# Kernel optimization log

Hardware: AMD Instinct MI355X
Metric: run time of the kernel (lower is better)

The kernel has to match this reference:

```python
import jax, jax.numpy as jnp
import numpy as np

B, T, D, NC = 2048, 16, 2048, 174
DH = D // 2
EPS = 1e-5


def setup_inputs() -> dict:
    key = jax.random.key(0)
    ks = jax.random.split(key, 10)
    std = 0.01
    return {
        "x": jax.random.normal(ks[0], (B, T, D), dtype=jnp.float32),
        "theta_w": jax.random.normal(ks[1], (DH, D), dtype=jnp.float32) * std,
        "phi_w": jax.random.normal(ks[2], (DH, D), dtype=jnp.float32) * std,
        "g_w": jax.random.normal(ks[3], (DH, D), dtype=jnp.float32) * std,
        "W_w": jax.random.normal(ks[4], (D, DH), dtype=jnp.float32) * std,
        "bn_gamma": jnp.ones((D,), dtype=jnp.float32),
        "bn_beta": jnp.zeros((D,), dtype=jnp.float32),
        "bn_mean": jax.random.normal(ks[5], (D,), dtype=jnp.float32) * 0.1,
        "bn_var": jax.random.uniform(ks[6], (D,), dtype=jnp.float32, minval=0.5, maxval=1.5),
        "fc1_w": jax.random.normal(ks[7], (512, T * D), dtype=jnp.float32) * 0.01,
        "fc1_b": jnp.zeros((512,), dtype=jnp.float32),
        "fc2_w": jax.random.normal(ks[8], (NC, 512), dtype=jnp.float32) * 0.01,
        "fc2_b": jnp.zeros((NC,), dtype=jnp.float32),
    }


def _bn(x_bdt, gamma, beta, mean, var):
    # inference-mode BatchNorm1d over channel dim D of [B, D, T]
    inv = gamma / jnp.sqrt(var + EPS)
    return x_bdt * inv[None, :, None] + (beta - mean * inv)[None, :, None]


def _attention_net(x_btd, theta_w, phi_w, g_w, W_w, bn):
    x_bdt = x_btd.reshape(B, D, T)  # torch .view semantics (reshape, not transpose)
    theta_x = jnp.einsum('od,bdt->bot', theta_w, x_bdt)  # [B, DH, T]
    phi_x = jnp.einsum('od,bdt->bot', phi_w, x_bdt)
    g_x = jnp.einsum('od,bdt->bot', g_w, x_bdt)
    scores = jnp.einsum('bot,bos->bts', theta_x, phi_x) / DH  # [B, T, T]
    alpha = jax.nn.softmax(scores, axis=-1)  # dropout is identity in eval
    context = jnp.einsum('bts,bos->bto', alpha, g_x)  # [B, T, DH]
    ctx = jnp.einsum('do,bto->bdt', W_w, context)  # W 1x1 conv -> [B, D, T]
    ctx = _bn(ctx, *bn)
    ctx = ctx.reshape(B, T, D)  # view(B, shape[-1], shape[-2])
    return ctx + x_btd


def _residual_block(x_bdt, theta_w, phi_w, g_w, W_w, bn):
    y = x_bdt
    h = _bn(x_bdt, *bn)
    h = h.reshape(B, T, D)
    h = _attention_net(h, theta_w, phi_w, g_w, W_w, bn)
    h = h.reshape(B, D, T)
    h = _bn(h, *bn)
    return h + y


def reference(x, theta_w, phi_w, g_w, W_w, bn_gamma, bn_beta, bn_mean, bn_var,
              fc1_w, fc1_b, fc2_w, fc2_b):
    bn = (bn_gamma, bn_beta, bn_mean, bn_var)
    skip = x  # [B, T, D]
    h = x.reshape(B, D, T)
    for _ in range(T):  # num_frames residual blocks (shared weights)
        h = _residual_block(h, theta_w, phi_w, g_w, W_w, bn)
    h = _bn(h, *bn)
    h = h.reshape(B, T, D) + skip
    h = h.reshape(B, T * D)
    h = jax.nn.relu(h)
    h = jax.nn.relu(h @ fc1_w.T + fc1_b)  # trn dropout identity in eval
    return h @ fc2_w.T + fc2_b  # [B, num_class]
```

## Files before the change

### kernel.cpp

```cpp
#include <hip/hip_runtime.h>
#include <math.h>
#include <stdint.h>


typedef float  floatx4 __attribute__((ext_vector_type(4)));
typedef float  floatx2 __attribute__((ext_vector_type(2)));
typedef _Float16 half8 __attribute__((ext_vector_type(8)));
typedef short  short8 __attribute__((ext_vector_type(8)));
typedef unsigned short ushort2v __attribute__((ext_vector_type(2)));
typedef unsigned short ushort4v __attribute__((ext_vector_type(4)));

#define BIGK (1 << 28)

__device__ __forceinline__ unsigned short h_bits(_Float16 h) {
  return __builtin_bit_cast(unsigned short, h);
}

__device__ __forceinline__ void gld_lds16(const unsigned short* g, unsigned short* l) {
  __builtin_amdgcn_global_load_lds(
      (const __attribute__((address_space(1))) unsigned int*)g,
      (__attribute__((address_space(3))) unsigned int*)l, 16, 0, 0);
}

template <int EPI>
__global__ __launch_bounds__(256, 2)
void gemm_f16(const unsigned short* __restrict__ A, int lda, int kfA,
              const unsigned short* __restrict__ B, int ldb, int kfB,
              int K, float* __restrict__ out0, unsigned short* __restrict__ out1,
              int ldo, const float* __restrict__ tbl,
              float cmult, float uscale, int writeU, long zAB, long zO) {
  __shared__ unsigned short As[128 * 64];
  __shared__ unsigned short Bs[128 * 64];
  if (zAB) { A += (long)blockIdx.z * zAB; B += (long)blockIdx.z * zAB; }
  if (zO) { out0 += (long)blockIdx.z * zO; }
  const int tid = threadIdx.x;
  const int w = tid >> 6, l = tid & 63;
  const int quad = l >> 4, lr = l & 15;
  const int m0 = blockIdx.x * 128, n0 = blockIdx.y * 128;
  const int wm = (w & 1) * 64, wn = (w >> 1) * 64;
  const int lsw = lr & 7;

  floatx4 acc[4][4];
#pragma unroll
  for (int a = 0; a < 4; a++)
#pragma unroll
    for (int b = 0; b < 4; b++)
#pragma unroll
      for (int q = 0; q < 4; q++) acc[a][b][q] = 0.f;

  for (int k0 = 0; k0 < K; k0 += 64) {
    int ka = (k0 >= kfA) ? k0 - kfA : k0;
    int kb = (k0 >= kfB) ? k0 - kfB : k0;
    __syncthreads();
#pragma unroll
    for (int i = 0; i < 4; i++) {
      int c = i * 256 + tid;
      int m = c >> 3;
      int kc = ((c & 7) ^ (m & 7)) * 8;
      gld_lds16(A + (size_t)(m0 + m) * lda + ka + kc, As + c * 8);
      gld_lds16(B + (size_t)(n0 + m) * ldb + kb + kc, Bs + c * 8);
    }
    __syncthreads();
#pragma unroll
    for (int kk = 0; kk < 64; kk += 32) {
      const int kq = (kk >> 3) + quad;
      const int ksw = (kq ^ lsw) * 8;
      short8 af[4], bf[4];
#pragma unroll
      for (int mi = 0; mi < 4; mi++)
        af[mi] = *(const short8*)(As + (wm + mi * 16 + lr) * 64 + ksw);
#pragma unroll
      for (int ni = 0; ni < 4; ni++)
        bf[ni] = *(const short8*)(Bs + (wn + ni * 16 + lr) * 64 + ksw);
#pragma unroll
      for (int mi = 0; mi < 4; mi++)
#pragma unroll
        for (int ni = 0; ni < 4; ni++)
          acc[mi][ni] = __builtin_amdgcn_mfma_f32_16x16x32_f16(
              __builtin_bit_cast(half8, af[mi]),
              __builtin_bit_cast(half8, bf[ni]), acc[mi][ni], 0, 0, 0);
    }
  }

  if (EPI == 0) {
#pragma unroll
    for (int mi = 0; mi < 4; mi++)
#pragma unroll
      for (int i2 = 0; i2 < 4; i2++) {
        int row = m0 + wm + mi * 16 + quad * 4 + i2;
#pragma unroll
        for (int ni = 0; ni < 4; ni++) {
          int col = n0 + wn + ni * 16 + lr;
          out0[(size_t)row * ldo + col] = acc[mi][ni][i2];
        }
      }
  } else {
    float invv[4], bb[4];
#pragma unroll
    for (int ni = 0; ni < 4; ni++) {
      int d = n0 + wn + ni * 16 + lr;
      invv[ni] = tbl[d];
      bb[ni] = tbl[2048 + d];
    }
#pragma unroll
    for (int mi = 0; mi < 4; mi++)
#pragma unroll
      for (int i2 = 0; i2 < 4; i2++) {
        size_t row = (size_t)(m0 + wm + mi * 16 + quad * 4 + i2);
#pragma unroll
        for (int ni = 0; ni < 4; ni++) {
          int d = n0 + wn + ni * 16 + lr;
          size_t off = row * (size_t)ldo + d;
          float hold = out0[off];
          float ctxv = acc[mi][ni][i2] * cmult;
          float u = __fadd_rn(__fmul_rn(hold, invv[ni]), bb[ni]);
          float cb = __fadd_rn(__fmul_rn(ctxv, invv[ni]), bb[ni]);
          float o1 = __fadd_rn(cb, u);
          float h2 = __fadd_rn(__fmul_rn(o1, invv[ni]), bb[ni]);
          float hn = __fadd_rn(h2, hold);
          out0[off] = hn;
          float un = __fadd_rn(__fmul_rn(hn, invv[ni]), bb[ni]);
          acc[mi][ni][i2] = un * uscale;
        }
      }
    if (writeU) {
      unsigned short* st = (w < 2) ? (As + w * 4096) : (Bs + (w - 2) * 4096);
      __syncthreads();
#pragma unroll
      for (int mi = 0; mi < 4; mi++)
#pragma unroll
        for (int i2 = 0; i2 < 4; i2++) {
          int rr = mi * 16 + quad * 4 + i2;
#pragma unroll
          for (int ni = 0; ni < 4; ni++)
            st[rr * 64 + ni * 16 + lr] = h_bits((_Float16)acc[mi][ni][i2]);
        }
      __syncthreads();
#pragma unroll
      for (int j = 0; j < 8; j++) {
        int chk = j * 64 + l, rr = chk >> 3, c8 = (chk & 7) * 8;
        short8 v = *(const short8*)(st + rr * 64 + c8);
        *(short8*)(out1 + (size_t)(m0 + wm + rr) * (2 * ldo) + n0 + wn + c8) = v;
      }
      __syncthreads();
#pragma unroll
      for (int mi = 0; mi < 4; mi++)
#pragma unroll
        for (int i2 = 0; i2 < 4; i2++) {
          int rr = mi * 16 + quad * 4 + i2;
#pragma unroll
          for (int ni = 0; ni < 4; ni++) {
            float u = acc[mi][ni][i2];
            _Float16 hh = (_Float16)u;
            st[rr * 64 + ni * 16 + lr] = h_bits((_Float16)(u - (float)hh));
          }
        }
      __syncthreads();
#pragma unroll
      for (int j = 0; j < 8; j++) {
        int chk = j * 64 + l, rr = chk >> 3, c8 = (chk & 7) * 8;
        short8 v = *(const short8*)(st + rr * 64 + c8);
        *(short8*)(out1 + (size_t)(m0 + wm + rr) * (2 * ldo) + ldo + n0 + wn + c8) = v;
      }
    }
  }
}

__global__ __launch_bounds__(256)
void attn_kernel(const float* __restrict__ TPG, unsigned short* __restrict__ ctx,
                 int Nn, float smult, float gmult, float scmult) {
  __shared__ float sTh[128 * 16];
  __shared__ float sPh[128 * 16];
  __shared__ float sGc[128 * 17];
  __shared__ float sS[256];
  __shared__ float sA[256];
  const int b = blockIdx.x, tid = threadIdx.x;
  const int t = tid >> 4, s = tid & 15;
  double acc = 0.0;
  for (int cc = 0; cc < 8; cc++) {
#pragma unroll
    for (int i = 0; i < 2; i++) {
      int fi = i * 256 + tid, r = fi >> 2, c = (fi & 3) * 4;
      *(floatx4*)&sTh[r * 16 + c] =
          *(const floatx4*)&TPG[(size_t)(cc * 128 + r) * Nn + b * 16 + c];
      *(floatx4*)&sPh[r * 16 + c] =
          *(const floatx4*)&TPG[(size_t)(1024 + cc * 128 + r) * Nn + b * 16 + c];
    }
    __syncthreads();
    for (int o = 0; o < 128; o++)
      acc += (double)sTh[o * 16 + t] * (double)sPh[o * 16 + s];
    __syncthreads();
  }
  float sv = (float)(acc * (double)smult);
  sS[tid] = sv;
  __syncthreads();
  float mx = sS[t * 16];
#pragma unroll
  for (int j = 1; j < 16; j++) mx = fmaxf(mx, sS[t * 16 + j]);
  float e = expf(sv - mx);
  sA[tid] = e;
  __syncthreads();
  float sum = 0.f;
#pragma unroll
  for (int j = 0; j < 16; j++) sum += sA[t * 16 + j];
  float alpha = e / sum;
  __syncthreads();
  sA[tid] = alpha;
  __syncthreads();
  const int t2 = tid >> 7, ol = tid & 127;
  for (int cc = 0; cc < 8; cc++) {
#pragma unroll
    for (int i = 0; i < 2; i++) {
      int fi = i * 256 + tid, r = fi >> 2, c = (fi & 3) * 4;
      floatx4 g = *(const floatx4*)&TPG[(size_t)(2048 + cc * 128 + r) * Nn + b * 16 + c];
      sGc[r * 17 + c + 0] = g[0] * gmult;
      sGc[r * 17 + c + 1] = g[1] * gmult;
      sGc[r * 17 + c + 2] = g[2] * gmult;
      sGc[r * 17 + c + 3] = g[3] * gmult;
    }
    __syncthreads();
#pragma unroll
    for (int tt = 0; tt < 8; tt++) {
      int tc = t2 + tt * 2;
      float cv = 0.f;
#pragma unroll
      for (int s2 = 0; s2 < 16; s2++) cv += sA[tc * 16 + s2] * sGc[ol * 17 + s2];
      float cs = cv * scmult;
      _Float16 chh = (_Float16)cs;
      _Float16 cll = (_Float16)(cs - (float)chh);
      size_t base = ((size_t)b * 16 + tc) * 2048 + cc * 128 + ol;
      ctx[base] = h_bits(chh);
      ctx[base + 1024] = h_bits(cll);
    }
    __syncthreads();
  }
}

__global__ __launch_bounds__(256)
void e0_kernel(const float* __restrict__ x, float* __restrict__ h,
               unsigned short* __restrict__ u2, const float* __restrict__ tbl,
               int b0, float uscale) {
  __shared__ float sx[16 * 129];
  const int bl = blockIdx.x, d0 = blockIdx.y * 128, tid = threadIdx.x;
  const float* xb = x + (size_t)(b0 + bl) * 32768;
#pragma unroll
  for (int i = 0; i < 2; i++) {
    int fi = i * 256 + tid, r = fi >> 2, c = (fi & 3) * 4;
    floatx4 v = *(const floatx4*)&xb[(d0 + r) * 16 + c];
    sx[(c + 0) * 129 + r] = v[0];
    sx[(c + 1) * 129 + r] = v[1];
    sx[(c + 2) * 129 + r] = v[2];
    sx[(c + 3) * 129 + r] = v[3];
  }
  __syncthreads();
  const int t4 = tid >> 6, dl = (tid & 63) * 2;
#pragma unroll
  for (int i = 0; i < 4; i++) {
    int t = t4 * 4 + i;
    int d = d0 + dl;
    float x0 = sx[t * 129 + dl], x1 = sx[t * 129 + dl + 1];
    size_t n = (size_t)bl * 16 + t;
    floatx2 hv; hv[0] = x0; hv[1] = x1;
    *(floatx2*)&h[n * 2048 + d] = hv;
    float i0 = tbl[d], i1 = tbl[d + 1], q0 = tbl[2048 + d], q1 = tbl[2048 + d + 1];
    float u0 = __fadd_rn(__fmul_rn(x0, i0), q0) * uscale;
    float u1 = __fadd_rn(__fmul_rn(x1, i1), q1) * uscale;
    _Float16 a0 = (_Float16)u0, a1 = (_Float16)u1;
    ushort2v uv; uv[0] = h_bits(a0); uv[1] = h_bits(a1);
    *(ushort2v*)&u2[n * 4096 + d] = uv;
    ushort2v lv;
    lv[0] = h_bits((_Float16)(u0 - (float)a0));
    lv[1] = h_bits((_Float16)(u1 - (float)a1));
    *(ushort2v*)&u2[n * 4096 + 2048 + d] = lv;
  }
}

__global__ __launch_bounds__(256)
void f1_kernel(const float* __restrict__ x, const float* __restrict__ h,
               unsigned short* __restrict__ r, const float* __restrict__ tbl, int b0) {
  __shared__ float sx[16 * 129];
  const int bl = blockIdx.x, d0 = blockIdx.y * 128, tid = threadIdx.x;
  const float* xb = x + (size_t)(b0 + bl) * 32768;
#pragma unroll
  for (int i = 0; i < 2; i++) {
    int fi = i * 256 + tid, rr = fi >> 2, c = (fi & 3) * 4;
    floatx4 v = *(const floatx4*)&xb[(d0 + rr) * 16 + c];
    sx[(c + 0) * 129 + rr] = v[0];
    sx[(c + 1) * 129 + rr] = v[1];
    sx[(c + 2) * 129 + rr] = v[2];
    sx[(c + 3) * 129 + rr] = v[3];
  }
  __syncthreads();
  const int t4 = tid >> 6, dl = (tid & 63) * 2;
#pragma unroll
  for (int i = 0; i < 4; i++) {
    int t = t4 * 4 + i;
    int d = d0 + dl;
    size_t n = (size_t)bl * 16 + t;
    floatx2 hv = *(const floatx2*)&h[n * 2048 + d];
    float i0 = tbl[d], i1 = tbl[d + 1], q0 = tbl[2048 + d], q1 = tbl[2048 + d + 1];
    float v0 = __fadd_rn(__fadd_rn(__fmul_rn(hv[0], i0), q0), sx[t * 129 + dl]);
    float v1 = __fadd_rn(__fadd_rn(__fmul_rn(hv[1], i1), q1), sx[t * 129 + dl + 1]);
    v0 = fmaxf(v0, 0.f);
    v1 = fmaxf(v1, 0.f);
    ushort2v rv;
    rv[0] = h_bits((_Float16)(v0 * 0x1p-14f));
    rv[1] = h_bits((_Float16)(v1 * 0x1p-14f));
    *(ushort2v*)&r[(size_t)(b0 + bl) * 32768 + (size_t)t * 2048 + d] = rv;
  }
}

__global__ __launch_bounds__(256)
void prep_tbl(const float* __restrict__ g, const float* __restrict__ be,
              const float* __restrict__ me, const float* __restrict__ va,
              float* __restrict__ tbl) {
  int d = blockIdx.x * 256 + threadIdx.x;
  if (d < 2048) {
    float inv = g[d] / sqrtf(va[d] + 1e-5f);
    tbl[d] = inv;
    tbl[2048 + d] = __fsub_rn(be[d], __fmul_rn(me[d], inv));
  }
}

__global__ __launch_bounds__(256)
void prep_qkv(const float* __restrict__ th, const float* __restrict__ ph,
              const float* __restrict__ gw, unsigned short* __restrict__ A1w) {
  int i = (blockIdx.x * 256 + threadIdx.x) * 4;
  int row = i >> 11, d = i & 2047;
  const float* src = (row < 1024) ? (th + (size_t)row * 2048 + d)
                   : (row < 2048) ? (ph + (size_t)(row - 1024) * 2048 + d)
                                  : (gw + (size_t)(row - 2048) * 2048 + d);
  floatx4 v = *(const floatx4*)src;
  ushort4v hi, lo;
#pragma unroll
  for (int j = 0; j < 4; j++) {
    float sc = v[j] * 4096.f;
    _Float16 hh = (_Float16)sc;
    hi[j] = h_bits(hh);
    lo[j] = h_bits((_Float16)(sc - (float)hh));
  }
  size_t base = (size_t)row * 6144 + d;
  *(ushort4v*)&A1w[base] = hi;
  *(ushort4v*)&A1w[base + 2048] = hi;
  *(ushort4v*)&A1w[base + 4096] = lo;
}

__global__ __launch_bounds__(256)
void prep_wc(const float* __restrict__ Ww, unsigned short* __restrict__ Wc6) {
  int i = (blockIdx.x * 256 + threadIdx.x) * 4;
  int row = i >> 10, o = i & 1023;
  floatx4 v = *(const floatx4*)&Ww[(size_t)row * 1024 + o];
  ushort4v hi, lo;
#pragma unroll
  for (int j = 0; j < 4; j++) {
    float sc = v[j] * 4096.f;
    _Float16 hh = (_Float16)sc;
    hi[j] = h_bits(hh);
    lo[j] = h_bits((_Float16)(sc - (float)hh));
  }
  size_t base = (size_t)row * 3072 + o;
  *(ushort4v*)&Wc6[base] = hi;
  *(ushort4v*)&Wc6[base + 1024] = hi;
  *(ushort4v*)&Wc6[base + 2048] = lo;
}

__global__ __launch_bounds__(256)
void prep_w1p(const float* __restrict__ w1, unsigned short* __restrict__ w1p) {
  __shared__ float sx[16 * 129];
  const int oc = blockIdx.x, d0 = blockIdx.y * 128, tid = threadIdx.x;
  const float* wb = w1 + (size_t)oc * 32768;
#pragma unroll
  for (int i = 0; i < 2; i++) {
    int fi = i * 256 + tid, rr = fi >> 2, c = (fi & 3) * 4;
    floatx4 v = *(const floatx4*)&wb[(d0 + rr) * 16 + c];
    sx[(c + 0) * 129 + rr] = v[0];
    sx[(c + 1) * 129 + rr] = v[1];
    sx[(c + 2) * 129 + rr] = v[2];
    sx[(c + 3) * 129 + rr] = v[3];
  }
  __syncthreads();
  const int t4 = tid >> 6, dl = (tid & 63) * 2;
#pragma unroll
  for (int i = 0; i < 4; i++) {
    int t = t4 * 4 + i, d = d0 + dl;
    ushort2v wv;
    wv[0] = h_bits((_Float16)sx[t * 129 + dl]);
    wv[1] = h_bits((_Float16)sx[t * 129 + dl + 1]);
    *(ushort2v*)&w1p[(size_t)oc * 32768 + (size_t)t * 2048 + d] = wv;
  }
}

__global__ __launch_bounds__(256)
void prep_w2t(const float* __restrict__ w2, float* __restrict__ w2t) {
  int o = blockIdx.x, tid = threadIdx.x;
  if (tid < 174) w2t[(size_t)o * 174 + tid] = w2[(size_t)tid * 512 + o];
}

__global__ __launch_bounds__(256)
void fc1red(const float* __restrict__ p, const float* __restrict__ b1,
            float* __restrict__ r1) {
  int i = blockIdx.x * 256 + threadIdx.x;
  int o = i & 511;
  const size_t S = (size_t)2048 * 512;
  float v = p[i] + p[i + S] + p[i + 2 * S] + p[i + 3 * S];
  v = v * 16384.f + b1[o];
  r1[i] = fmaxf(v, 0.f);
}

__global__ __launch_bounds__(256)
void fc2_kernel(const float* __restrict__ r1, const float* __restrict__ w2t,
                const float* __restrict__ b2, float* __restrict__ out) {
  __shared__ float sR[512];
  const int b = blockIdx.x, tid = threadIdx.x;
  sR[tid] = r1[(size_t)b * 512 + tid];
  sR[tid + 256] = r1[(size_t)b * 512 + tid + 256];
  __syncthreads();
  if (tid < 174) {
    float a = b2[tid];
    for (int o = 0; o < 512; o++) a += sR[o] * w2t[o * 174 + tid];
    out[(size_t)b * 174 + tid] = a;
  }
}

extern "C" void kernel_launch(void* const* d_in, const int* in_sizes, int n_in,
                              void* d_out, int out_size, void* d_ws, size_t ws_size,
                              hipStream_t stream) {
  const float* x = (const float*)d_in[0];
  const float* thw = (const float*)d_in[1];
  const float* phw = (const float*)d_in[2];
  const float* gw = (const float*)d_in[3];
  const float* Ww = (const float*)d_in[4];
  const float* gam = (const float*)d_in[5];
  const float* bet = (const float*)d_in[6];
  const float* mea = (const float*)d_in[7];
  const float* var = (const float*)d_in[8];
  const float* w1 = (const float*)d_in[9];
  const float* b1 = (const float*)d_in[10];
  const float* w2 = (const float*)d_in[11];
  const float* b2 = (const float*)d_in[12];

  auto AL = [](size_t v) { return (v + 255) & ~(size_t)255; };
  const size_t fixed = AL((size_t)2048 * 32768 * 2)
                     + AL((size_t)3072 * 6144 * 2)
                     + AL((size_t)2048 * 3072 * 2)
                     + AL((size_t)512 * 32768 * 2)
                     + AL((size_t)4 * 2048 * 512 * 4)
                     + AL((size_t)2048 * 512 * 4)
                     + AL((size_t)512 * 174 * 4)
                     + AL((size_t)4096 * 4);
  int nsplit = 16;
  for (int cand : {1, 2, 4, 8, 16}) {
    size_t Nn_ = (size_t)32768 / cand;
    size_t per = AL(Nn_ * 2048 * 4) + AL(Nn_ * 4096 * 2) +
                 AL((size_t)3072 * Nn_ * 4) + AL(Nn_ * 2048 * 2);
    if (fixed + per <= ws_size) { nsplit = cand; break; }
  }
  const int Nb = 2048 / nsplit;
  const int Nn = Nb * 16;

  char* pp = (char*)d_ws;
  auto take = [&](size_t n) { char* q = pp; pp += (n + 255) & ~(size_t)255; return q; };
  unsigned short* rbuf = (unsigned short*)take((size_t)2048 * 32768 * 2);
  unsigned short* A1w = (unsigned short*)take((size_t)3072 * 6144 * 2);
  unsigned short* Wc6 = (unsigned short*)take((size_t)2048 * 3072 * 2);
  unsigned short* w1p = (unsigned short*)take((size_t)512 * 32768 * 2);
  float* r1p = (float*)take((size_t)4 * 2048 * 512 * 4);
  float* r1 = (float*)take((size_t)2048 * 512 * 4);
  float* w2t = (float*)take((size_t)512 * 174 * 4);
  float* tbl = (float*)take((size_t)4096 * 4);
  float* h = (float*)take((size_t)Nn * 2048 * 4);
  unsigned short* u2 = (unsigned short*)take((size_t)Nn * 4096 * 2);
  float* TPG = (float*)take((size_t)3072 * Nn * 4);
  unsigned short* ctxb = (unsigned short*)take((size_t)Nn * 2048 * 2);

  static const int ks[17] = {0, 0, 0, 0, 0, 0, 0, 0, 2, 3, 5, 7, 8, 10, 11, 13, 15};

  prep_tbl<<<8, 256, 0, stream>>>(gam, bet, mea, var, tbl);
  prep_qkv<<<6144, 256, 0, stream>>>(thw, phw, gw, A1w);
  prep_wc<<<2048, 256, 0, stream>>>(Ww, Wc6);
  prep_w1p<<<dim3(512, 16), 256, 0, stream>>>(w1, w1p);
  prep_w2t<<<512, 256, 0, stream>>>(w2, w2t);

  for (int sp = 0; sp < nsplit; sp++) {
    int b0 = sp * Nb;
    e0_kernel<<<dim3(Nb, 16), 256, 0, stream>>>(x, h, u2, tbl, b0, 1.0f);
    for (int it = 0; it < 16; it++) {
      gemm_f16<0><<<dim3(24, Nn / 128), 256, 0, stream>>>(
          A1w, 6144, BIGK, u2, 4096, 4096, 6144, TPG, nullptr, Nn, nullptr,
          0.f, 0.f, 0, 0, 0);
      attn_kernel<<<dim3(Nb), 256, 0, stream>>>(
          TPG, ctxb, Nn,
          ldexpf(1.f, 2 * ks[it] - 34),
          ldexpf(1.f, ks[it] - 12),
          ldexpf(1.f, -ks[it] - 2));
      gemm_f16<2><<<dim3(Nn / 128, 16), 256, 0, stream>>>(
          ctxb, 2048, 2048, Wc6, 3072, BIGK, 3072, h, u2, 2048, tbl,
          ldexpf(1.f, ks[it] - 10),
          ldexpf(1.f, -ks[it + 1]),
          (it < 15) ? 1 : 0, 0, 0);
    }
    f1_kernel<<<dim3(Nb, 16), 256, 0, stream>>>(x, h, rbuf, tbl, b0);
  }

  gemm_f16<0><<<dim3(16, 4, 4), 256, 0, stream>>>(
      rbuf, 32768, BIGK, w1p, 32768, BIGK, 8192, r1p, nullptr, 512, nullptr,
      0.f, 0.f, 0, 8192, (long)2048 * 512);
  fc1red<<<4096, 256, 0, stream>>>(r1p, b1, r1);
  fc2_kernel<<<2048, 256, 0, stream>>>(r1, w2t, b2, (float*)d_out);
}
```

Before: 31.63 ms.

## Load hi/lo fp16 split operands once and issue three MFMA products per tile

The split-precision GEMMs previously emulated the three hi*hi + hi*lo + lo*hi products by concatenating duplicated hi/lo weight copies along K (6144/3072-wide). Now the GEMM loads A-hi, A-lo, B-hi and B-lo tiles for each 32-wide K step into four LDS buffers and issues the three MFMA products directly. This removes the duplicated weight storage and the redundant global loads of the duplicated hi copies. It also shrinks the K-step to 32 with a new swizzle, which means more barriers per unit of work.

```diff
diff --git a/kernel.cpp b/kernel.cpp
--- a/kernel.cpp
+++ b/kernel.cpp
@@ -10,8 +10,6 @@
 typedef unsigned short ushort2v __attribute__((ext_vector_type(2)));
 typedef unsigned short ushort4v __attribute__((ext_vector_type(4)));
 
-#define BIGK (1 << 28)
-
 __device__ __forceinline__ unsigned short h_bits(_Float16 h) {
   return __builtin_bit_cast(unsigned short, h);
 }
@@ -22,15 +20,18 @@
       (__attribute__((address_space(3))) unsigned int*)l, 16, 0, 0);
 }
 
-template <int EPI>
+#define MFMA16(a, b, c) \
+  __builtin_amdgcn_mfma_f32_16x16x32_f16( \
+      __builtin_bit_cast(half8, a), __builtin_bit_cast(half8, b), c, 0, 0, 0)
+
+template <int TERMS, int EPI>
 __global__ __launch_bounds__(256, 2)
-void gemm_f16(const unsigned short* __restrict__ A, int lda, int kfA,
-              const unsigned short* __restrict__ B, int ldb, int kfB,
-              int K, float* __restrict__ out0, unsigned short* __restrict__ out1,
+void gemm_f16(const unsigned short* __restrict__ A, int lda,
+              const unsigned short* __restrict__ B, int ldb,
+              int K2, float* __restrict__ out0, unsigned short* __restrict__ out1,
               int ldo, const float* __restrict__ tbl,
               float cmult, float uscale, int writeU, long zAB, long zO) {
-  __shared__ unsigned short As[128 * 64];
-  __shared__ unsigned short Bs[128 * 64];
+  __shared__ unsigned short sm[4][128 * 32];
   if (zAB) { A += (long)blockIdx.z * zAB; B += (long)blockIdx.z * zAB; }
   if (zO) { out0 += (long)blockIdx.z * zO; }
   const int tid = threadIdx.x;
@@ -38,7 +39,6 @@
   const int quad = l >> 4, lr = l & 15;
   const int m0 = blockIdx.x * 128, n0 = blockIdx.y * 128;
   const int wm = (w & 1) * 64, wn = (w >> 1) * 64;
-  const int lsw = lr & 7;
 
   floatx4 acc[4][4];
 #pragma unroll
@@ -48,37 +48,82 @@
 #pragma unroll
       for (int q = 0; q < 4; q++) acc[a][b][q] = 0.f;
 
-  for (int k0 = 0; k0 < K; k0 += 64) {
-    int ka = (k0 >= kfA) ? k0 - kfA : k0;
-    int kb = (k0 >= kfB) ? k0 - kfB : k0;
-    __syncthreads();
-#pragma unroll
-    for (int i = 0; i < 4; i++) {
-      int c = i * 256 + tid;
-      int m = c >> 3;
-      int kc = ((c & 7) ^ (m & 7)) * 8;
-      gld_lds16(A + (size_t)(m0 + m) * lda + ka + kc, As + c * 8);
-      gld_lds16(B + (size_t)(n0 + m) * ldb + kb + kc, Bs + c * 8);
-    }
-    __syncthreads();
-#pragma unroll
-    for (int kk = 0; kk < 64; kk += 32) {
-      const int kq = (kk >> 3) + quad;
-      const int ksw = (kq ^ lsw) * 8;
-      short8 af[4], bf[4];
+  if (TERMS == 3) {
+    const unsigned short* Alo = A + K2;
+    const unsigned short* Blo = B + K2;
+    const int fsw = (quad ^ ((lr >> 1) & 3)) * 8;
+    for (int k0 = 0; k0 < K2; k0 += 32) {
+      __syncthreads();
+#pragma unroll
+      for (int i = 0; i < 2; i++) {
+        int c = i * 256 + tid;
+        int m = c >> 2;
+        int cs = ((c & 3) ^ ((m >> 1) & 3)) * 8;
+        gld_lds16(A + (size_t)(m0 + m) * lda + k0 + cs, &sm[0][0] + c * 8);
+        gld_lds16(Alo + (size_t)(m0 + m) * lda + k0 + cs, &sm[1][0] + c * 8);
+        gld_lds16(B + (size_t)(n0 + m) * ldb + k0 + cs, &sm[2][0] + c * 8);
+        gld_lds16(Blo + (size_t)(n0 + m) * ldb + k0 + cs, &sm[3][0] + c * 8);
+      }
+      __syncthreads();
+      short8 ah[4], bh[4], al[4], bl[4];
+#pragma unroll
+      for (int mi = 0; mi < 4; mi++) {
+        ah[mi] = *(const short8*)(&sm[0][0] + (wm + mi * 16 + lr) * 32 + fsw);
+        al[mi] = *(const short8*)(&sm[1][0] + (wm + mi * 16 + lr) * 32 + fsw);
+      }
+#pragma unroll
+      for (int ni = 0; ni < 4; ni++) {
+        bh[ni] = *(const short8*)(&sm[2][0] + (wn + ni * 16 + lr) * 32 + fsw);
+        bl[ni] = *(const short8*)(&sm[3][0] + (wn + ni * 16 + lr) * 32 + fsw);
+      }
 #pragma unroll
       for (int mi = 0; mi < 4; mi++)
-        af[mi] = *(const short8*)(As + (wm + mi * 16 + lr) * 64 + ksw);
-#pragma unroll
-      for (int ni = 0; ni < 4; ni++)
-        bf[ni] = *(const short8*)(Bs + (wn + ni * 16 + lr) * 64 + ksw);
+#pragma unroll
+        for (int ni = 0; ni < 4; ni++)
+          acc[mi][ni] = MFMA16(ah[mi], bh[ni], acc[mi][ni]);
 #pragma unroll
       for (int mi = 0; mi < 4; mi++)
 #pragma unroll
         for (int ni = 0; ni < 4; ni++)
-          acc[mi][ni] = __builtin_amdgcn_mfma_f32_16x16x32_f16(
-              __builtin_bit_cast(half8, af[mi]),
-              __builtin_bit_cast(half8, bf[ni]), acc[mi][ni], 0, 0, 0);
+          acc[mi][ni] = MFMA16(ah[mi], bl[ni], acc[mi][ni]);
+#pragma unroll
+      for (int mi = 0; mi < 4; mi++)
+#pragma unroll
+        for (int ni = 0; ni < 4; ni++)
+          acc[mi][ni] = MFMA16(al[mi], bh[ni], acc[mi][ni]);
+    }
+  } else {
+    unsigned short* As = &sm[0][0];
+    unsigned short* Bs = &sm[2][0];
+    const int lsw = lr & 7;
+    for (int k0 = 0; k0 < K2; k0 += 64) {
+      __syncthreads();
+#pragma unroll
+      for (int i = 0; i < 4; i++) {
+        int c = i * 256 + tid;
+        int m = c >> 3;
+        int kc = ((c & 7) ^ (m & 7)) * 8;
+        gld_lds16(A + (size_t)(m0 + m) * lda + k0 + kc, As + c * 8);
+        gld_lds16(B + (size_t)(n0 + m) * ldb + k0 + kc, Bs + c * 8);
+      }
+      __syncthreads();
+#pragma unroll
+      for (int kk = 0; kk < 64; kk += 32) {
+        const int kq = (kk >> 3) + quad;
+        const int ksw = (kq ^ lsw) * 8;
+        short8 af[4], bf[4];
+#pragma unroll
+        for (int mi = 0; mi < 4; mi++)
+          af[mi] = *(const short8*)(As + (wm + mi * 16 + lr) * 64 + ksw);
+#pragma unroll
+        for (int ni = 0; ni < 4; ni++)
+          bf[ni] = *(const short8*)(Bs + (wn + ni * 16 + lr) * 64 + ksw);
+#pragma unroll
+        for (int mi = 0; mi < 4; mi++)
+#pragma unroll
+          for (int ni = 0; ni < 4; ni++)
+            acc[mi][ni] = MFMA16(af[mi], bf[ni], acc[mi][ni]);
+      }
     }
   }
 
@@ -124,7 +169,7 @@
         }
       }
     if (writeU) {
-      unsigned short* st = (w < 2) ? (As + w * 4096) : (Bs + (w - 2) * 4096);
+      unsigned short* st = &sm[w][0];
       __syncthreads();
 #pragma unroll
       for (int mi = 0; mi < 4; mi++)
@@ -339,14 +384,13 @@
     hi[j] = h_bits(hh);
     lo[j] = h_bits((_Float16)(sc - (float)hh));
   }
-  size_t base = (size_t)row * 6144 + d;
+  size_t base = (size_t)row * 4096 + d;
   *(ushort4v*)&A1w[base] = hi;
-  *(ushort4v*)&A1w[base + 2048] = hi;
-  *(ushort4v*)&A1w[base + 4096] = lo;
-}
-
-__global__ __launch_bounds__(256)
-void prep_wc(const float* __restrict__ Ww, unsigned short* __restrict__ Wc6) {
+  *(ushort4v*)&A1w[base + 2048] = lo;
+}
+
+__global__ __launch_bounds__(256)
+void prep_wc(const float* __restrict__ Ww, unsigned short* __restrict__ Wc2) {
   int i = (blockIdx.x * 256 + threadIdx.x) * 4;
   int row = i >> 10, o = i & 1023;
   floatx4 v = *(const floatx4*)&Ww[(size_t)row * 1024 + o];
@@ -358,10 +402,9 @@
     hi[j] = h_bits(hh);
     lo[j] = h_bits((_Float16)(sc - (float)hh));
   }
-  size_t base = (size_t)row * 3072 + o;
-  *(ushort4v*)&Wc6[base] = hi;
-  *(ushort4v*)&Wc6[base + 1024] = hi;
-  *(ushort4v*)&Wc6[base + 2048] = lo;
+  size_t base = (size_t)row * 2048 + o;
+  *(ushort4v*)&Wc2[base] = hi;
+  *(ushort4v*)&Wc2[base + 1024] = lo;
 }
 
 __global__ __launch_bounds__(256)
@@ -441,8 +484,8 @@
 
   auto AL = [](size_t v) { return (v + 255) & ~(size_t)255; };
   const size_t fixed = AL((size_t)2048 * 32768 * 2)
-                     + AL((size_t)3072 * 6144 * 2)
-                     + AL((size_t)2048 * 3072 * 2)
+                     + AL((size_t)3072 * 4096 * 2)
+                     + AL((size_t)2048 * 2048 * 2)
                      + AL((size_t)512 * 32768 * 2)
                      + AL((size_t)4 * 2048 * 512 * 4)
                      + AL((size_t)2048 * 512 * 4)
@@ -461,8 +504,8 @@
   char* pp = (char*)d_ws;
   auto take = [&](size_t n) { char* q = pp; pp += (n + 255) & ~(size_t)255; return q; };
   unsigned short* rbuf = (unsigned short*)take((size_t)2048 * 32768 * 2);
-  unsigned short* A1w = (unsigned short*)take((size_t)3072 * 6144 * 2);
-  unsigned short* Wc6 = (unsigned short*)take((size_t)2048 * 3072 * 2);
+  unsigned short* A1w = (unsigned short*)take((size_t)3072 * 4096 * 2);
+  unsigned short* Wc2 = (unsigned short*)take((size_t)2048 * 2048 * 2);
   unsigned short* w1p = (unsigned short*)take((size_t)512 * 32768 * 2);
   float* r1p = (float*)take((size_t)4 * 2048 * 512 * 4);
   float* r1 = (float*)take((size_t)2048 * 512 * 4);
@@ -477,7 +520,7 @@
 
   prep_tbl<<<8, 256, 0, stream>>>(gam, bet, mea, var, tbl);
   prep_qkv<<<6144, 256, 0, stream>>>(thw, phw, gw, A1w);
-  prep_wc<<<2048, 256, 0, stream>>>(Ww, Wc6);
+  prep_wc<<<2048, 256, 0, stream>>>(Ww, Wc2);
   prep_w1p<<<dim3(512, 16), 256, 0, stream>>>(w1, w1p);
   prep_w2t<<<512, 256, 0, stream>>>(w2, w2t);
 
@@ -485,16 +528,16 @@
     int b0 = sp * Nb;
     e0_kernel<<<dim3(Nb, 16), 256, 0, stream>>>(x, h, u2, tbl, b0, 1.0f);
     for (int it = 0; it < 16; it++) {
-      gemm_f16<0><<<dim3(24, Nn / 128), 256, 0, stream>>>(
-          A1w, 6144, BIGK, u2, 4096, 4096, 6144, TPG, nullptr, Nn, nullptr,
+      gemm_f16<3, 0><<<dim3(24, Nn / 128), 256, 0, stream>>>(
+          A1w, 4096, u2, 4096, 2048, TPG, nullptr, Nn, nullptr,
           0.f, 0.f, 0, 0, 0);
       attn_kernel<<<dim3(Nb), 256, 0, stream>>>(
           TPG, ctxb, Nn,
           ldexpf(1.f, 2 * ks[it] - 34),
           ldexpf(1.f, ks[it] - 12),
           ldexpf(1.f, -ks[it] - 2));
-      gemm_f16<2><<<dim3(Nn / 128, 16), 256, 0, stream>>>(
-          ctxb, 2048, 2048, Wc6, 3072, BIGK, 3072, h, u2, 2048, tbl,
+      gemm_f16<3, 2><<<dim3(Nn / 128, 16), 256, 0, stream>>>(
+          ctxb, 2048, Wc2, 2048, 1024, h, u2, 2048, tbl,
           ldexpf(1.f, ks[it] - 10),
           ldexpf(1.f, -ks[it + 1]),
           (it < 15) ? 1 : 0, 0, 0);
@@ -502,8 +545,8 @@
     f1_kernel<<<dim3(Nb, 16), 256, 0, stream>>>(x, h, rbuf, tbl, b0);
   }
 
-  gemm_f16<0><<<dim3(16, 4, 4), 256, 0, stream>>>(
-      rbuf, 32768, BIGK, w1p, 32768, BIGK, 8192, r1p, nullptr, 512, nullptr,
+  gemm_f16<1, 0><<<dim3(16, 4, 4), 256, 0, stream>>>(
+      rbuf, 32768, w1p, 32768, 8192, r1p, nullptr, 512, nullptr,
       0.f, 0.f, 0, 8192, (long)2048 * 512);
   fc1red<<<4096, 256, 0, stream>>>(r1p, b1, r1);
   fc2_kernel<<<2048, 256, 0, stream>>>(r1, w2t, b2, (float*)d_out);
```

Result: no change. 31.01 ms (-1.9%).
